# Kernel tuning notes

Measured on AMD Instinct MI355X. Metric: run time of the kernel, lower is better.

Reference implementation:

```python
import jax, jax.numpy as jnp
import numpy as np

B, S, E, HEADS = 2, 2048, 2048, 16


def setup_inputs() -> dict:
    key = jax.random.key(0)
    k1, k2, k3 = jax.random.split(key, 3)
    x = jax.random.normal(k1, (B, S, E), dtype=jnp.float32)
    # Linear weights stored as (in, out); torch uses y = x @ W.T with W (out, in) -- same math.
    W_qkvh = jax.random.normal(k2, (E, 3 * E + HEADS), dtype=jnp.float32) * (E ** -0.5)
    W_out = jax.random.normal(k3, (E, E), dtype=jnp.float32) * (E ** -0.5)
    return {"x": x, "W_qkvh": W_qkvh, "W_out": W_out}


def reference(x, W_qkvh, W_out):
    b, s, e = x.shape
    heads = W_qkvh.shape[1] - 3 * e
    d = e // heads
    scale = e ** 0.5

    proj = x @ W_qkvh                                  # (b, s, 3e + heads)
    QKV, Hg = proj[..., : 3 * e], proj[..., 3 * e:]
    Hg = jnp.tanh(Hg).transpose(0, 2, 1)[..., None]    # (b, h, s, 1) gate
    QKV = QKV.reshape(b, s, heads, 3 * d).transpose(0, 2, 1, 3)  # (b, h, s, 3d)
    Q, K, V = jnp.split(QKV, 3, axis=-1)               # each (b, h, s, d)

    # Cummean(H*K) along seq: cumsum(n * x) / n^2 with n = 1..s
    n = jnp.arange(1, s + 1, dtype=x.dtype).reshape(1, 1, s, 1)
    Kc = jnp.cumsum(n * (Hg * K), axis=2) / (n * n)    # (b, h, s, d)

    scores = jnp.einsum('bhqd,bhkd->bhqk', Q, Kc) / scale
    causal = jnp.triu(jnp.ones((s, s), dtype=bool), k=1)
    scores = jnp.where(causal, -jnp.inf, scores)
    attn = jax.nn.softmax(scores, axis=-1)

    out = jnp.einsum('bhqk,bhkd->bhqd', attn, V)       # (b, h, s, d)
    out = out.transpose(0, 2, 1, 3).reshape(b, s, e)
    return out @ W_out
```

## Files before the change

### kernel.cpp

```cpp
#include <hip/hip_runtime.h>
#include <hip/hip_bf16.h>
#include <math.h>

#define PB 2
#define PS 2048
#define PE 2048
#define PH 16
#define PD 128
#define PN_PROJ 6160
#define PM 4096
#define PQKV 6144

typedef __attribute__((ext_vector_type(8))) short bf16x8;
typedef __attribute__((ext_vector_type(4))) float f32x4;

__device__ __forceinline__ void gload_lds16(const void* g, void* l) {
  __builtin_amdgcn_global_load_lds((const __attribute__((address_space(1))) void*)g,
                                   (__attribute__((address_space(3))) void*)l, 16, 0, 0);
}

template <int BM, int BN, int WM, int WN, typename OutT>
__global__ __launch_bounds__(512, 1) void gemm_cs2(
    const __hip_bfloat16* __restrict__ A, const __hip_bfloat16* __restrict__ Bt,
    OutT* __restrict__ C, int K, int lda, int ldb, int ldc, int nTilesX) {
  constexpr int MF = BM / WM / 16;
  constexpr int NF = BN / WN / 16;
  constexpr int SLOT = (BM + BN) * 64;
  constexpr int AL = BM / 64;
  constexpr int BL = BN / 64;
  constexpr int NLD = AL + BL;

  __shared__ __align__(16) __hip_bfloat16 lds[2 * SLOT];

  const int tid = threadIdx.x;
  const int w = tid >> 6, lane = tid & 63;
  const int fq = lane >> 4, fr = lane & 15;
  const int wm = w / WN, wn = w % WN;

  const int total = gridDim.x;
  const int swz = (blockIdx.x & 7) * (total >> 3) + (blockIdx.x >> 3);
  const int mBase = (swz / nTilesX) * BM;
  const int nBase = (swz % nTilesX) * BN;

  const int srow = tid >> 3, sc = tid & 7;

  auto stage = [&](int t) {
    char* base = (char*)lds + (size_t)(t & 1) * SLOT * 2;
#pragma unroll
    for (int l = 0; l < AL; ++l) {
      int row = l * 64 + srow;
      int cs = sc ^ (row & 7);
      gload_lds16(A + (size_t)(mBase + row) * lda + t * 64 + cs * 8,
                  base + l * 8192 + w * 1024);
    }
#pragma unroll
    for (int l = 0; l < BL; ++l) {
      int row = l * 64 + srow;
      int cs = sc ^ (row & 7);
      gload_lds16(Bt + (size_t)(nBase + row) * ldb + t * 64 + cs * 8,
                  base + BM * 128 + l * 8192 + w * 1024);
    }
  };

  f32x4 acc[MF][NF];
#pragma unroll
  for (int m = 0; m < MF; ++m)
#pragma unroll
    for (int n = 0; n < NF; ++n) acc[m][n] = (f32x4){0.f, 0.f, 0.f, 0.f};

  const int NT = K / 64;
  stage(0); stage(1);

#pragma unroll 1
  for (int t = 0; t < NT; ++t) {
    if (t + 1 < NT) asm volatile("s_waitcnt vmcnt(%0)" ::"i"(NLD) : "memory");
    else            asm volatile("s_waitcnt vmcnt(0)" ::: "memory");
    __builtin_amdgcn_s_barrier();
    __builtin_amdgcn_sched_barrier(0);

    const __hip_bfloat16* sl = lds + (size_t)(t & 1) * SLOT;

    bf16x8 av[MF], bv[NF];
#pragma unroll
    for (int m = 0; m < MF; ++m) {
      int row = wm * (BM / WM) + m * 16 + fr;
      av[m] = *(const bf16x8*)&sl[row * 64 + ((fq ^ (row & 7)) * 8)];
    }
#pragma unroll
    for (int n = 0; n < NF; ++n) {
      int row = wn * (BN / WN) + n * 16 + fr;
      bv[n] = *(const bf16x8*)&sl[BM * 64 + row * 64 + ((fq ^ (row & 7)) * 8)];
    }
    asm volatile("s_waitcnt lgkmcnt(0)" ::: "memory");
    __builtin_amdgcn_sched_barrier(0);
    __builtin_amdgcn_s_setprio(1);
#pragma unroll
    for (int m = 0; m < MF; ++m)
#pragma unroll
      for (int n = 0; n < NF; ++n)
        acc[m][n] = __builtin_amdgcn_mfma_f32_16x16x32_bf16(av[m], bv[n], acc[m][n], 0, 0, 0);
    __builtin_amdgcn_s_setprio(0);

#pragma unroll
    for (int m = 0; m < MF; ++m) {
      int row = wm * (BM / WM) + m * 16 + fr;
      av[m] = *(const bf16x8*)&sl[row * 64 + (((4 + fq) ^ (row & 7)) * 8)];
    }
#pragma unroll
    for (int n = 0; n < NF; ++n) {
      int row = wn * (BN / WN) + n * 16 + fr;
      bv[n] = *(const bf16x8*)&sl[BM * 64 + row * 64 + (((4 + fq) ^ (row & 7)) * 8)];
    }
    asm volatile("s_waitcnt lgkmcnt(0)" ::: "memory");
    __builtin_amdgcn_s_barrier();
    __builtin_amdgcn_sched_barrier(0);
    if (t + 2 < NT) stage(t + 2);
    __builtin_amdgcn_s_setprio(1);
#pragma unroll
    for (int m = 0; m < MF; ++m)
#pragma unroll
      for (int n = 0; n < NF; ++n)
        acc[m][n] = __builtin_amdgcn_mfma_f32_16x16x32_bf16(av[m], bv[n], acc[m][n], 0, 0, 0);
    __builtin_amdgcn_s_setprio(0);
  }

#pragma unroll
  for (int m = 0; m < MF; ++m) {
#pragma unroll
    for (int n = 0; n < NF; ++n) {
      int row0 = mBase + wm * (BM / WM) + m * 16 + fq * 4;
      int col = nBase + wn * (BN / WN) + n * 16 + fr;
#pragma unroll
      for (int j = 0; j < 4; ++j) {
        if constexpr (__is_same(OutT, float))
          C[(size_t)(row0 + j) * ldc + col] = acc[m][n][j];
        else
          C[(size_t)(row0 + j) * ldc + col] = __float2bfloat16(acc[m][n][j]);
      }
    }
  }
}

template <int BM, int BN, int WM, int WN, typename OutT>
__global__ __launch_bounds__(512, 1) void gemm_cs3(
    const __hip_bfloat16* __restrict__ A, const __hip_bfloat16* __restrict__ Bt,
    OutT* __restrict__ C, int K, int lda, int ldb, int ldc, int nTilesX) {
  constexpr int MF = BM / WM / 16;
  constexpr int NF = BN / WN / 16;
  constexpr int SLOT = (BM + BN) * 64;
  constexpr int AL = BM / 64;
  constexpr int BL = BN / 64;
  constexpr int NLD = AL + BL;

  __shared__ __align__(16) __hip_bfloat16 lds[3 * SLOT];

  const int tid = threadIdx.x;
  const int w = tid >> 6, lane = tid & 63;
  const int fq = lane >> 4, fr = lane & 15;
  const int wm = w / WN, wn = w % WN;

  const int total = gridDim.x;
  const int swz = (blockIdx.x & 7) * (total >> 3) + (blockIdx.x >> 3);
  const int mBase = (swz / nTilesX) * BM;
  const int nBase = (swz % nTilesX) * BN;

  const int srow = tid >> 3, sc = tid & 7;

  auto stage = [&](int t) {
    char* base = (char*)lds + (size_t)(t % 3) * SLOT * 2;
#pragma unroll
    for (int l = 0; l < AL; ++l) {
      int row = l * 64 + srow;
      int cs = sc ^ (row & 7);
      gload_lds16(A + (size_t)(mBase + row) * lda + t * 64 + cs * 8,
                  base + l * 8192 + w * 1024);
    }
#pragma unroll
    for (int l = 0; l < BL; ++l) {
      int row = l * 64 + srow;
      int cs = sc ^ (row & 7);
      gload_lds16(Bt + (size_t)(nBase + row) * ldb + t * 64 + cs * 8,
                  base + BM * 128 + l * 8192 + w * 1024);
    }
  };

  f32x4 acc[MF][NF];
#pragma unroll
  for (int m = 0; m < MF; ++m)
#pragma unroll
    for (int n = 0; n < NF; ++n) acc[m][n] = (f32x4){0.f, 0.f, 0.f, 0.f};

  const int NT = K / 64;
  stage(0); stage(1);

#pragma unroll 1
  for (int t = 0; t < NT; ++t) {
    if (t + 1 < NT) asm volatile("s_waitcnt vmcnt(%0)" ::"i"(NLD) : "memory");
    else            asm volatile("s_waitcnt vmcnt(0)" ::: "memory");
    __builtin_amdgcn_s_barrier();
    __builtin_amdgcn_sched_barrier(0);
    if (t + 2 < NT) stage(t + 2);

    const __hip_bfloat16* sl = lds + (size_t)(t % 3) * SLOT;

#pragma unroll
    for (int kk = 0; kk < 2; ++kk) {
      bf16x8 av[MF], bv[NF];
#pragma unroll
      for (int m = 0; m < MF; ++m) {
        int row = wm * (BM / WM) + m * 16 + fr;
        av[m] = *(const bf16x8*)&sl[row * 64 + (((kk * 4 + fq) ^ (row & 7)) * 8)];
      }
#pragma unroll
      for (int n = 0; n < NF; ++n) {
        int row = wn * (BN / WN) + n * 16 + fr;
        bv[n] = *(const bf16x8*)&sl[BM * 64 + row * 64 + (((kk * 4 + fq) ^ (row & 7)) * 8)];
      }
      asm volatile("s_waitcnt lgkmcnt(0)" ::: "memory");
      __builtin_amdgcn_sched_barrier(0);
      __builtin_amdgcn_s_setprio(1);
#pragma unroll
      for (int m = 0; m < MF; ++m)
#pragma unroll
        for (int n = 0; n < NF; ++n)
          acc[m][n] = __builtin_amdgcn_mfma_f32_16x16x32_bf16(av[m], bv[n], acc[m][n], 0, 0, 0);
      __builtin_amdgcn_s_setprio(0);
    }
  }

#pragma unroll
  for (int m = 0; m < MF; ++m) {
#pragma unroll
    for (int n = 0; n < NF; ++n) {
      int row0 = mBase + wm * (BM / WM) + m * 16 + fq * 4;
      int col = nBase + wn * (BN / WN) + n * 16 + fr;
#pragma unroll
      for (int j = 0; j < 4; ++j) {
        if constexpr (__is_same(OutT, float))
          C[(size_t)(row0 + j) * ldc + col] = acc[m][n][j];
        else
          C[(size_t)(row0 + j) * ldc + col] = __float2bfloat16(acc[m][n][j]);
      }
    }
  }
}

__global__ __launch_bounds__(256) void cast_f32_bf16(const float* __restrict__ in,
                                                     __hip_bfloat16* __restrict__ out,
                                                     int n4) {
  int i = blockIdx.x * 256 + threadIdx.x;
  if (i >= n4) return;
  float4 v = ((const float4*)in)[i];
  union { __hip_bfloat16 h[4]; uint2 u; } pk;
  pk.h[0] = __float2bfloat16(v.x); pk.h[1] = __float2bfloat16(v.y);
  pk.h[2] = __float2bfloat16(v.z); pk.h[3] = __float2bfloat16(v.w);
  ((uint2*)out)[i] = pk.u;
}

__global__ __launch_bounds__(256) void transpose_cast(const float* __restrict__ W,
                                                      __hip_bfloat16* __restrict__ Wt,
                                                      int ldw, int ldt, int nOff) {
  __shared__ float t[32][33];
  int nb = blockIdx.x * 32, kb = blockIdx.y * 32;
  int tx = threadIdx.x & 31, ty = threadIdx.x >> 5;
#pragma unroll
  for (int i = 0; i < 4; ++i) {
    int k = ty + i * 8;
    t[k][tx] = W[(size_t)(kb + k) * ldw + nOff + nb + tx];
  }
  __syncthreads();
#pragma unroll
  for (int i = 0; i < 4; ++i) {
    int n = ty + i * 8;
    Wt[(size_t)(nb + n) * ldt + kb + tx] = __float2bfloat16(t[tx][n]);
  }
}

__global__ __launch_bounds__(256) void hg_from_x(const float* __restrict__ x,
                                                 const float* __restrict__ W,
                                                 float* __restrict__ hgbuf) {
  int bs = blockIdx.x;
  int b = bs >> 11, s = bs & (PS - 1);
  __shared__ float xs[PE];
  __shared__ float red[16][17];
  const float* xr = x + (size_t)bs * PE;
  for (int i = threadIdx.x; i < PE / 4; i += 256)
    *(float4*)&xs[i * 4] = ((const float4*)xr)[i];
  __syncthreads();
  int h = threadIdx.x & 15, part = threadIdx.x >> 4;
  float acc = 0.f;
  for (int k = part * 128; k < part * 128 + 128; ++k)
    acc += xs[k] * W[(size_t)k * PN_PROJ + 3 * PE + h];
  red[part][h] = acc;
  __syncthreads();
  if (threadIdx.x < 16) {
    float sm = 0.f;
#pragma unroll
    for (int p = 0; p < 16; ++p) sm += red[p][threadIdx.x];
    hgbuf[(size_t)(b * PH + threadIdx.x) * PS + s] = tanhf(sm);
  }
}

#define KC_SCALE 0.022097086912079608f

__global__ __launch_bounds__(128) void kc_pass1(const __hip_bfloat16* __restrict__ proj,
                                                const float* __restrict__ hgbuf,
                                                float* __restrict__ csum) {
  int c = blockIdx.x & 15, bh = blockIdx.x >> 4;
  int h = bh & (PH - 1), b = bh >> 4;
  int d = threadIdx.x;
  __shared__ float hgs[128];
  hgs[d] = hgbuf[bh * PS + c * 128 + d];
  __syncthreads();
  const __hip_bfloat16* kbase = proj + (size_t)(b * PS) * PQKV + h * 384 + 128 + d;
  float acc = 0.f;
  int j0 = c * 128;
  for (int i = 0; i < 128; ++i) {
    int j = j0 + i;
    acc += (float)(j + 1) * hgs[i] * __bfloat162float(kbase[(size_t)j * PQKV]);
  }
  csum[blockIdx.x * 128 + d] = acc;
}

__global__ __launch_bounds__(128) void kc_pass2(__hip_bfloat16* __restrict__ proj,
                                                const float* __restrict__ hgbuf,
                                                const float* __restrict__ csum) {
  int c = blockIdx.x & 15, bh = blockIdx.x >> 4;
  int h = bh & (PH - 1), b = bh >> 4;
  int d = threadIdx.x;
  __shared__ float hgs[128];
  hgs[d] = hgbuf[bh * PS + c * 128 + d];
  __syncthreads();
  float acc = 0.f;
  for (int cc = 0; cc < c; ++cc) acc += csum[(bh * 16 + cc) * 128 + d];
  __hip_bfloat16* kbase = proj + (size_t)(b * PS) * PQKV + h * 384 + 128 + d;
  int j0 = c * 128;
  for (int i = 0; i < 128; ++i) {
    int j = j0 + i;
    acc += (float)(j + 1) * hgs[i] * __bfloat162float(kbase[(size_t)j * PQKV]);
    float t = (float)(j + 1);
    kbase[(size_t)j * PQKV] = __float2bfloat16(acc / (t * t) * KC_SCALE);
  }
}

__global__ __launch_bounds__(256) void vt_pack(const __hip_bfloat16* __restrict__ proj,
                                               __hip_bfloat16* __restrict__ Vtp) {
  int sc = blockIdx.x & 31, bh = blockIdx.x >> 5;
  int b = bh >> 4, h = bh & 15;
  int s0 = sc * 64;
  int tid = threadIdx.x;
  __shared__ __align__(16) __hip_bfloat16 Vlds[64][136];
  const __hip_bfloat16* src = proj + (size_t)(b * PS + s0) * PQKV + h * 384 + 256;
#pragma unroll
  for (int it = 0; it < 4; ++it) {
    int i = it * 256 + tid;
    int row = i >> 4, ch = i & 15;
    *(bf16x8*)&Vlds[row][ch * 8] = *(const bf16x8*)&src[(size_t)row * PQKV + ch * 8];
  }
  __syncthreads();
  int d = tid >> 1, half = tid & 1;
  __hip_bfloat16* dst = Vtp + ((size_t)bh * 128 + d) * PS + s0 + half * 32;
#pragma unroll
  for (int c8 = 0; c8 < 8; ++c8) {
    union { __hip_bfloat16 h4[4]; uint2 u; } pk;
#pragma unroll
    for (int k = 0; k < 4; ++k) pk.h4[k] = Vlds[half * 32 + c8 * 4 + k][d];
    *(uint2*)&dst[c8 * 4] = pk.u;
  }
}

__global__ __launch_bounds__(256) void attn_mfma(const __hip_bfloat16* __restrict__ proj,
                                                 const __hip_bfloat16* __restrict__ Vtp,
                                                 __hip_bfloat16* __restrict__ O) {
  const int bid = (blockIdx.x & 7) * 32 + (blockIdx.x >> 3);
  const int bh = bid >> 3, pk = bid & 7;
  const int b = bh >> 4, h = bh & 15;
  const int tid = threadIdx.x;
  const int w = tid >> 6, lane = tid & 63;
  const int fq = lane >> 4, fr = lane & 15;

  __shared__ __align__(16) char smem[120832];
  __hip_bfloat16* Psw = (__hip_bfloat16*)(smem + 65536) + w * 32 * 72;
  __hip_bfloat16* Os = (__hip_bfloat16*)(smem + 84480);

  const __hip_bfloat16* kb0 = proj + (size_t)(b * PS) * PQKV + h * 384 + 128;
  const __hip_bfloat16* vb0 = Vtp + (size_t)bh * 128 * PS;

  const int klr = lane >> 4, kc = lane & 15;
  const int vlr = lane >> 3, vc = lane & 7;

  auto stageKV = [&](int t, int bufi) {
    char* ksb = smem + bufi * 16384;
    char* vsb = smem + 32768 + bufi * 16384;
    const __hip_bfloat16* kb = kb0 + (size_t)(t * 64) * PQKV;
    const __hip_bfloat16* vb = vb0 + t * 64;
#pragma unroll
    for (int p = 0; p < 4; ++p) {
      int row = w * 16 + p * 4 + klr;
      int cs = kc ^ (row & 7);
      gload_lds16(kb + (size_t)row * PQKV + cs * 8, ksb + (w * 16 + p * 4) * 256);
    }
#pragma unroll
    for (int p = 0; p < 4; ++p) {
      int row = w * 32 + p * 8 + vlr;
      int cs = vc ^ (row & 7);
      gload_lds16(vb + (size_t)row * PS + cs * 8, vsb + (w * 32 + p * 8) * 128);
    }
  };

  stageKV(0, 0);
  int cur = 0;

#pragma unroll 1
  for (int phase = 0; phase < 2; ++phase) {
    const int qt = (phase == 0) ? pk : 15 - pk;
    const int nt = (qt + 1) * 2;
    const int q0 = qt * 128;
    const int qw = q0 + w * 32;

    const __hip_bfloat16* qbase = proj + (size_t)(b * PS + qw) * PQKV + h * 384;
    bf16x8 qf[2][4];
#pragma unroll
    for (int r2 = 0; r2 < 2; ++r2)
#pragma unroll
      for (int kk = 0; kk < 4; ++kk)
        qf[r2][kk] = *(const bf16x8*)&qbase[(size_t)(r2 * 16 + fr) * PQKV + kk * 32 + fq * 8];

    f32x4 oacc[2][8];
#pragma unroll
    for (int r2 = 0; r2 < 2; ++r2)
#pragma unroll
      for (int nd = 0; nd < 8; ++nd) oacc[r2][nd] = (f32x4){0.f, 0.f, 0.f, 0.f};
    float m_[2] = {-__builtin_inff(), -__builtin_inff()};
    float l_[2] = {0.f, 0.f};

#pragma unroll 1
    for (int kt = 0; kt < nt; ++kt) {
      const bool hasNext = (kt + 1 < nt) || (phase == 0);
      if (hasNext) stageKV((kt + 1 < nt) ? kt + 1 : 0, cur ^ 1);

      if (kt * 64 <= qw + 31) {
        const __hip_bfloat16* Ks = (const __hip_bfloat16*)(smem + cur * 16384);
        const __hip_bfloat16* Vts = (const __hip_bfloat16*)(smem + 32768 + cur * 16384);
        const bool diag = (kt * 64 + 63) > qw;

        f32x4 sacc[2][4];
#pragma unroll
        for (int r2 = 0; r2 < 2; ++r2)
#pragma unroll
          for (int n = 0; n < 4; ++n) sacc[r2][n] = (f32x4){0.f, 0.f, 0.f, 0.f};
#pragma unroll
        for (int kk = 0; kk < 4; ++kk) {
#pragma unroll
          for (int n = 0; n < 4; ++n) {
            bf16x8 kf = *(const bf16x8*)&Ks[(n * 16 + fr) * 128 + (((kk * 4 + fq) ^ (fr & 7)) * 8)];
            sacc[0][n] = __builtin_amdgcn_mfma_f32_16x16x32_bf16(kf, qf[0][kk], sacc[0][n], 0, 0, 0);
            sacc[1][n] = __builtin_amdgcn_mfma_f32_16x16x32_bf16(kf, qf[1][kk], sacc[1][n], 0, 0, 0);
          }
        }

#pragma unroll
        for (int r2 = 0; r2 < 2; ++r2) {
          const int qg = qw + r2 * 16 + fr;
          float sv[4][4];
#pragma unroll
          for (int n = 0; n < 4; ++n)
#pragma unroll
            for (int j = 0; j < 4; ++j) {
              float s = sacc[r2][n][j];
              if (diag && (kt * 64 + n * 16 + fq * 4 + j) > qg) s = -__builtin_inff();
              sv[n][j] = s;
            }
          float pmax = sv[0][0];
#pragma unroll
          for (int n = 0; n < 4; ++n)
#pragma unroll
            for (int j = 0; j < 4; ++j) pmax = fmaxf(pmax, sv[n][j]);
          pmax = fmaxf(pmax, __shfl_xor(pmax, 16, 64));
          pmax = fmaxf(pmax, __shfl_xor(pmax, 32, 64));

          const bool nof = __all(pmax <= m_[r2] + 8.f);
          const float mn = nof ? m_[r2] : fmaxf(m_[r2], pmax);
          float ps = 0.f;
#pragma unroll
          for (int n = 0; n < 4; ++n) {
            union { __hip_bfloat16 hh[4]; uint2 u; } pkk;
#pragma unroll
            for (int j = 0; j < 4; ++j) {
              float p = __expf(sv[n][j] - mn);
              ps += p;
              pkk.hh[j] = __float2bfloat16(p);
            }
            *(uint2*)&Psw[(r2 * 16 + fr) * 72 + n * 16 + fq * 4] = pkk.u;
          }
          ps += __shfl_xor(ps, 16, 64);
          ps += __shfl_xor(ps, 32, 64);

          if (!nof) {
            const float alpha = __expf(m_[r2] - mn);
            l_[r2] = l_[r2] * alpha + ps;
            m_[r2] = mn;
            float a0 = __shfl(alpha, fq * 4 + 0, 64);
            float a1 = __shfl(alpha, fq * 4 + 1, 64);
            float a2 = __shfl(alpha, fq * 4 + 2, 64);
            float a3 = __shfl(alpha, fq * 4 + 3, 64);
#pragma unroll
            for (int nd = 0; nd < 8; ++nd) {
              oacc[r2][nd][0] *= a0; oacc[r2][nd][1] *= a1;
              oacc[r2][nd][2] *= a2; oacc[r2][nd][3] *= a3;
            }
          } else {
            l_[r2] += ps;
          }
        }

#pragma unroll
        for (int kk2 = 0; kk2 < 2; ++kk2) {
          bf16x8 pa0 = *(const bf16x8*)&Psw[(0 * 16 + fr) * 72 + kk2 * 32 + fq * 8];
          bf16x8 pa1 = *(const bf16x8*)&Psw[(1 * 16 + fr) * 72 + kk2 * 32 + fq * 8];
#pragma unroll
          for (int nd = 0; nd < 8; ++nd) {
            bf16x8 vf = *(const bf16x8*)&Vts[(nd * 16 + fr) * 64 + (((kk2 * 4 + fq) ^ (fr & 7)) * 8)];
            oacc[0][nd] = __builtin_amdgcn_mfma_f32_16x16x32_bf16(pa0, vf, oacc[0][nd], 0, 0, 0);
            oacc[1][nd] = __builtin_amdgcn_mfma_f32_16x16x32_bf16(pa1, vf, oacc[1][nd], 0, 0, 0);
          }
        }
      }

      __syncthreads();
      cur ^= 1;
    }

    float i0 = 1.0f / l_[0], i1 = 1.0f / l_[1];
    float inv4[2][4];
#pragma unroll
    for (int j = 0; j < 4; ++j) {
      inv4[0][j] = __shfl(i0, fq * 4 + j, 64);
      inv4[1][j] = __shfl(i1, fq * 4 + j, 64);
    }
#pragma unroll
    for (int r2 = 0; r2 < 2; ++r2)
#pragma unroll
      for (int nd = 0; nd < 8; ++nd)
#pragma unroll
        for (int j = 0; j < 4; ++j)
          Os[(w * 32 + r2 * 16 + fq * 4 + j) * 136 + nd * 16 + fr] =
              __float2bfloat16(oacc[r2][nd][j] * inv4[r2][j]);
    __syncthreads();
#pragma unroll
    for (int it = 0; it < 8; ++it) {
      int i = it * 256 + tid;
      int row = i >> 4, ch = i & 15;
      *(bf16x8*)&O[(size_t)(b * PS + q0 + row) * PE + h * 128 + ch * 8] =
          *(const bf16x8*)&Os[row * 136 + ch * 8];
    }
  }
}

extern "C" void kernel_launch(void* const* d_in, const int* in_sizes, int n_in,
                              void* d_out, int out_size, void* d_ws, size_t ws_size,
                              hipStream_t stream) {
  const float* x     = (const float*)d_in[0];
  const float* Wqkvh = (const float*)d_in[1];
  const float* Wout  = (const float*)d_in[2];
  float* out = (float*)d_out;

  char* wsb = (char*)d_ws;
  __hip_bfloat16* proj = (__hip_bfloat16*)wsb;
  wsb += (size_t)PM * PQKV * 2;
  __hip_bfloat16* xb = (__hip_bfloat16*)wsb;
  wsb += (size_t)PM * PE * 2;
  __hip_bfloat16* Wq_t = (__hip_bfloat16*)wsb;
  wsb += (size_t)PQKV * PE * 2;
  __hip_bfloat16* Wout_t = (__hip_bfloat16*)wsb;
  wsb += (size_t)PE * PE * 2;
  __hip_bfloat16* Vtp = (__hip_bfloat16*)wsb;
  wsb += (size_t)PB * PH * PD * PS * 2;
  float* hgbuf = (float*)wsb;
  wsb += (size_t)PB * PH * PS * 4;
  float* csum = (float*)wsb;

  cast_f32_bf16<<<(PM * PE / 4 + 255) / 256, 256, 0, stream>>>(x, xb, PM * PE / 4);
  transpose_cast<<<dim3(PQKV / 32, PE / 32), 256, 0, stream>>>(Wqkvh, Wq_t, PN_PROJ, PE, 0);
  transpose_cast<<<dim3(PE / 32, PE / 32), 256, 0, stream>>>(Wout, Wout_t, PE, PE, 0);

  gemm_cs2<128, 384, 2, 4, __hip_bfloat16>
      <<<dim3((PM / 128) * (PQKV / 384)), 512, 0, stream>>>(
          xb, Wq_t, proj, PE, PE, PE, PQKV, PQKV / 384);

  hg_from_x<<<PM, 256, 0, stream>>>(x, Wqkvh, hgbuf);
  kc_pass1<<<PB * PH * 16, 128, 0, stream>>>(proj, hgbuf, csum);
  kc_pass2<<<PB * PH * 16, 128, 0, stream>>>(proj, hgbuf, csum);

  vt_pack<<<PB * PH * 32, 256, 0, stream>>>(proj, Vtp);
  __hip_bfloat16* Ob = xb;
  attn_mfma<<<PB * PH * 8, 256, 0, stream>>>(proj, Vtp, Ob);

  gemm_cs3<128, 256, 2, 4, float>
      <<<dim3((PM / 128) * (PE / 256)), 512, 0, stream>>>(
          Ob, Wout_t, out, PE, PE, PE, PE, PE / 256);
}
```

Baseline: 319.5 us.

## Replace QKV projection GEMM with 256x256 tile, four-phase ping-pong MFMA schedule

The QKV projection GEMM moves from a 128x384 tile to a 256x256 tile whose per-warp 128x64 sub-tile is processed in four quadrants. LDS fragment loads for the next quadrant are interleaved with MFMA bursts, separated by block barriers and setprio, in a ping-pong style. The aim is to raise arithmetic intensity per LDS byte and overlap LDS reads with matrix math. It uses the full 128KB of LDS and more barriers per k-step. The grid shrinks to 384 blocks, which may fill the CUs less evenly.

```diff
diff --git a/kernel.cpp b/kernel.cpp
--- a/kernel.cpp
+++ b/kernel.cpp
@@ -19,117 +19,150 @@
                                    (__attribute__((address_space(3))) void*)l, 16, 0, 0);
 }
 
-template <int BM, int BN, int WM, int WN, typename OutT>
-__global__ __launch_bounds__(512, 1) void gemm_cs2(
+template <typename OutT>
+__global__ __launch_bounds__(512, 1) void gemm_8p(
     const __hip_bfloat16* __restrict__ A, const __hip_bfloat16* __restrict__ Bt,
     OutT* __restrict__ C, int K, int lda, int ldb, int ldc, int nTilesX) {
-  constexpr int MF = BM / WM / 16;
-  constexpr int NF = BN / WN / 16;
-  constexpr int SLOT = (BM + BN) * 64;
-  constexpr int AL = BM / 64;
-  constexpr int BL = BN / 64;
-  constexpr int NLD = AL + BL;
-
-  __shared__ __align__(16) __hip_bfloat16 lds[2 * SLOT];
+  __shared__ __align__(16) char lds[131072];
 
   const int tid = threadIdx.x;
   const int w = tid >> 6, lane = tid & 63;
   const int fq = lane >> 4, fr = lane & 15;
-  const int wm = w / WN, wn = w % WN;
+  const int wm = w >> 2, wn = w & 3;
 
   const int total = gridDim.x;
   const int swz = (blockIdx.x & 7) * (total >> 3) + (blockIdx.x >> 3);
-  const int mBase = (swz / nTilesX) * BM;
-  const int nBase = (swz % nTilesX) * BN;
+  const int mBase = (swz / nTilesX) * 256;
+  const int nBase = (swz % nTilesX) * 256;
 
   const int srow = tid >> 3, sc = tid & 7;
 
   auto stage = [&](int t) {
-    char* base = (char*)lds + (size_t)(t & 1) * SLOT * 2;
-#pragma unroll
-    for (int l = 0; l < AL; ++l) {
+    char* base = lds + (size_t)(t & 1) * 65536;
+#pragma unroll
+    for (int l = 0; l < 4; ++l) {
       int row = l * 64 + srow;
       int cs = sc ^ (row & 7);
       gload_lds16(A + (size_t)(mBase + row) * lda + t * 64 + cs * 8,
                   base + l * 8192 + w * 1024);
     }
 #pragma unroll
-    for (int l = 0; l < BL; ++l) {
+    for (int l = 0; l < 4; ++l) {
       int row = l * 64 + srow;
       int cs = sc ^ (row & 7);
       gload_lds16(Bt + (size_t)(nBase + row) * ldb + t * 64 + cs * 8,
-                  base + BM * 128 + l * 8192 + w * 1024);
+                  base + 32768 + l * 8192 + w * 1024);
     }
   };
 
-  f32x4 acc[MF][NF];
-#pragma unroll
-  for (int m = 0; m < MF; ++m)
-#pragma unroll
-    for (int n = 0; n < NF; ++n) acc[m][n] = (f32x4){0.f, 0.f, 0.f, 0.f};
+  f32x4 acc[8][4];
+#pragma unroll
+  for (int m = 0; m < 8; ++m)
+#pragma unroll
+    for (int n = 0; n < 4; ++n) acc[m][n] = (f32x4){0.f, 0.f, 0.f, 0.f};
 
   const int NT = K / 64;
   stage(0); stage(1);
 
 #pragma unroll 1
   for (int t = 0; t < NT; ++t) {
-    if (t + 1 < NT) asm volatile("s_waitcnt vmcnt(%0)" ::"i"(NLD) : "memory");
+    if (t + 1 < NT) asm volatile("s_waitcnt vmcnt(8)" ::: "memory");
     else            asm volatile("s_waitcnt vmcnt(0)" ::: "memory");
     __builtin_amdgcn_s_barrier();
     __builtin_amdgcn_sched_barrier(0);
 
-    const __hip_bfloat16* sl = lds + (size_t)(t & 1) * SLOT;
-
-    bf16x8 av[MF], bv[NF];
-#pragma unroll
-    for (int m = 0; m < MF; ++m) {
-      int row = wm * (BM / WM) + m * 16 + fr;
-      av[m] = *(const bf16x8*)&sl[row * 64 + ((fq ^ (row & 7)) * 8)];
-    }
-#pragma unroll
-    for (int n = 0; n < NF; ++n) {
-      int row = wn * (BN / WN) + n * 16 + fr;
-      bv[n] = *(const bf16x8*)&sl[BM * 64 + row * 64 + ((fq ^ (row & 7)) * 8)];
-    }
+    const __hip_bfloat16* slA = (const __hip_bfloat16*)(lds + (size_t)(t & 1) * 65536);
+    const __hip_bfloat16* slB = slA + 16384;
+
+    bf16x8 avA[4][2], bv01[2][2], bv23[2][2], avB[4][2];
+#pragma unroll
+    for (int m = 0; m < 4; ++m)
+#pragma unroll
+      for (int kk = 0; kk < 2; ++kk) {
+        int row = wm * 128 + m * 16 + fr;
+        avA[m][kk] = *(const bf16x8*)&slA[row * 64 + (((kk * 4 + fq) ^ (row & 7)) * 8)];
+      }
+#pragma unroll
+    for (int n = 0; n < 2; ++n)
+#pragma unroll
+      for (int kk = 0; kk < 2; ++kk) {
+        int row = wn * 64 + n * 16 + fr;
+        bv01[n][kk] = *(const bf16x8*)&slB[row * 64 + (((kk * 4 + fq) ^ (row & 7)) * 8)];
+      }
+    __builtin_amdgcn_s_barrier();
     asm volatile("s_waitcnt lgkmcnt(0)" ::: "memory");
     __builtin_amdgcn_sched_barrier(0);
     __builtin_amdgcn_s_setprio(1);
 #pragma unroll
-    for (int m = 0; m < MF; ++m)
-#pragma unroll
-      for (int n = 0; n < NF; ++n)
-        acc[m][n] = __builtin_amdgcn_mfma_f32_16x16x32_bf16(av[m], bv[n], acc[m][n], 0, 0, 0);
+    for (int m = 0; m < 4; ++m)
+#pragma unroll
+      for (int n = 0; n < 2; ++n)
+#pragma unroll
+        for (int kk = 0; kk < 2; ++kk)
+          acc[m][n] = __builtin_amdgcn_mfma_f32_16x16x32_bf16(avA[m][kk], bv01[n][kk], acc[m][n], 0, 0, 0);
     __builtin_amdgcn_s_setprio(0);
-
-#pragma unroll
-    for (int m = 0; m < MF; ++m) {
-      int row = wm * (BM / WM) + m * 16 + fr;
-      av[m] = *(const bf16x8*)&sl[row * 64 + (((4 + fq) ^ (row & 7)) * 8)];
-    }
-#pragma unroll
-    for (int n = 0; n < NF; ++n) {
-      int row = wn * (BN / WN) + n * 16 + fr;
-      bv[n] = *(const bf16x8*)&sl[BM * 64 + row * 64 + (((4 + fq) ^ (row & 7)) * 8)];
-    }
+    __builtin_amdgcn_s_barrier();
+
+#pragma unroll
+    for (int n = 0; n < 2; ++n)
+#pragma unroll
+      for (int kk = 0; kk < 2; ++kk) {
+        int row = wn * 64 + (2 + n) * 16 + fr;
+        bv23[n][kk] = *(const bf16x8*)&slB[row * 64 + (((kk * 4 + fq) ^ (row & 7)) * 8)];
+      }
+    __builtin_amdgcn_s_barrier();
     asm volatile("s_waitcnt lgkmcnt(0)" ::: "memory");
-    __builtin_amdgcn_s_barrier();
     __builtin_amdgcn_sched_barrier(0);
+    __builtin_amdgcn_s_setprio(1);
+#pragma unroll
+    for (int m = 0; m < 4; ++m)
+#pragma unroll
+      for (int n = 0; n < 2; ++n)
+#pragma unroll
+        for (int kk = 0; kk < 2; ++kk)
+          acc[m][2 + n] = __builtin_amdgcn_mfma_f32_16x16x32_bf16(avA[m][kk], bv23[n][kk], acc[m][2 + n], 0, 0, 0);
+    __builtin_amdgcn_s_setprio(0);
+    __builtin_amdgcn_s_barrier();
+
+#pragma unroll
+    for (int m = 0; m < 4; ++m)
+#pragma unroll
+      for (int kk = 0; kk < 2; ++kk) {
+        int row = wm * 128 + (4 + m) * 16 + fr;
+        avB[m][kk] = *(const bf16x8*)&slA[row * 64 + (((kk * 4 + fq) ^ (row & 7)) * 8)];
+      }
+    __builtin_amdgcn_s_barrier();
+    asm volatile("s_waitcnt lgkmcnt(0)" ::: "memory");
+    __builtin_amdgcn_sched_barrier(0);
+    __builtin_amdgcn_s_setprio(1);
+#pragma unroll
+    for (int m = 0; m < 4; ++m)
+#pragma unroll
+      for (int n = 0; n < 2; ++n)
+#pragma unroll
+        for (int kk = 0; kk < 2; ++kk)
+          acc[4 + m][2 + n] = __builtin_amdgcn_mfma_f32_16x16x32_bf16(avB[m][kk], bv23[n][kk], acc[4 + m][2 + n], 0, 0, 0);
+    __builtin_amdgcn_s_setprio(0);
+    __builtin_amdgcn_s_barrier();
+
     if (t + 2 < NT) stage(t + 2);
     __builtin_amdgcn_s_setprio(1);
 #pragma unroll
-    for (int m = 0; m < MF; ++m)
-#pragma unroll
-      for (int n = 0; n < NF; ++n)
-        acc[m][n] = __builtin_amdgcn_mfma_f32_16x16x32_bf16(av[m], bv[n], acc[m][n], 0, 0, 0);
+    for (int m = 0; m < 4; ++m)
+#pragma unroll
+      for (int n = 0; n < 2; ++n)
+#pragma unroll
+        for (int kk = 0; kk < 2; ++kk)
+          acc[4 + m][n] = __builtin_amdgcn_mfma_f32_16x16x32_bf16(avB[m][kk], bv01[n][kk], acc[4 + m][n], 0, 0, 0);
     __builtin_amdgcn_s_setprio(0);
   }
 
 #pragma unroll
-  for (int m = 0; m < MF; ++m) {
-#pragma unroll
-    for (int n = 0; n < NF; ++n) {
-      int row0 = mBase + wm * (BM / WM) + m * 16 + fq * 4;
-      int col = nBase + wn * (BN / WN) + n * 16 + fr;
+  for (int m = 0; m < 8; ++m) {
+#pragma unroll
+    for (int n = 0; n < 4; ++n) {
+      int row0 = mBase + wm * 128 + m * 16 + fq * 4;
+      int col = nBase + wn * 64 + n * 16 + fr;
 #pragma unroll
       for (int j = 0; j < 4; ++j) {
         if constexpr (__is_same(OutT, float))
@@ -584,9 +617,9 @@
   transpose_cast<<<dim3(PQKV / 32, PE / 32), 256, 0, stream>>>(Wqkvh, Wq_t, PN_PROJ, PE, 0);
   transpose_cast<<<dim3(PE / 32, PE / 32), 256, 0, stream>>>(Wout, Wout_t, PE, PE, 0);
 
-  gemm_cs2<128, 384, 2, 4, __hip_bfloat16>
-      <<<dim3((PM / 128) * (PQKV / 384)), 512, 0, stream>>>(
-          xb, Wq_t, proj, PE, PE, PE, PQKV, PQKV / 384);
+  gemm_8p<__hip_bfloat16>
+      <<<dim3((PM / 256) * (PQKV / 256)), 512, 0, stream>>>(
+          xb, Wq_t, proj, PE, PE, PE, PQKV, PQKV / 256);
 
   hg_from_x<<<PM, 256, 0, stream>>>(x, Wqkvh, hgbuf);
   kc_pass1<<<PB * PH * 16, 128, 0, stream>>>(proj, hgbuf, csum);
```

Result: slower. 341.5 us (+6.9%).

## Write QKV projection head-major and fold x bf16 cast into gate kernel

Applied to the files above, without the earlier changes.

The QKV GEMM epilogue now scatters results into separate head-major Q, K and V buffers laid out (b,h,s,d), replacing the interleaved (b*s, 3E) projection matrix. Downstream kernels (cumsum passes, V transpose, attention) read contiguous 256-byte rows instead of rows strided by 6144 elements. Separately, the standalone f32-to-bf16 cast of x is removed and done inside hg_from_x, which already loads x into shared memory, saving one launch and one read of x. The GEMM epilogue store now has a per-element head/batch index computation and writes to three destinations.

```diff
diff --git a/kernel.cpp b/kernel.cpp
--- a/kernel.cpp
+++ b/kernel.cpp
@@ -9,7 +9,6 @@
 #define PD 128
 #define PN_PROJ 6160
 #define PM 4096
-#define PQKV 6144
 
 typedef __attribute__((ext_vector_type(8))) short bf16x8;
 typedef __attribute__((ext_vector_type(4))) float f32x4;
@@ -19,10 +18,11 @@
                                    (__attribute__((address_space(3))) void*)l, 16, 0, 0);
 }
 
-template <int BM, int BN, int WM, int WN, typename OutT>
-__global__ __launch_bounds__(512, 1) void gemm_cs2(
+__global__ __launch_bounds__(512, 1) void gemm_qkv(
     const __hip_bfloat16* __restrict__ A, const __hip_bfloat16* __restrict__ Bt,
-    OutT* __restrict__ C, int K, int lda, int ldb, int ldc, int nTilesX) {
+    __hip_bfloat16* __restrict__ Qp, __hip_bfloat16* __restrict__ Kp,
+    __hip_bfloat16* __restrict__ Vp, int K, int nTilesX) {
+  constexpr int BM = 128, BN = 384, WM = 2, WN = 4;
   constexpr int MF = BM / WM / 16;
   constexpr int NF = BN / WN / 16;
   constexpr int SLOT = (BM + BN) * 64;
@@ -40,7 +40,8 @@
   const int total = gridDim.x;
   const int swz = (blockIdx.x & 7) * (total >> 3) + (blockIdx.x >> 3);
   const int mBase = (swz / nTilesX) * BM;
-  const int nBase = (swz % nTilesX) * BN;
+  const int h = swz % nTilesX;
+  const int nBase = h * BN;
 
   const int srow = tid >> 3, sc = tid & 7;
 
@@ -50,14 +51,14 @@
     for (int l = 0; l < AL; ++l) {
       int row = l * 64 + srow;
       int cs = sc ^ (row & 7);
-      gload_lds16(A + (size_t)(mBase + row) * lda + t * 64 + cs * 8,
+      gload_lds16(A + (size_t)(mBase + row) * K + t * 64 + cs * 8,
                   base + l * 8192 + w * 1024);
     }
 #pragma unroll
     for (int l = 0; l < BL; ++l) {
       int row = l * 64 + srow;
       int cs = sc ^ (row & 7);
-      gload_lds16(Bt + (size_t)(nBase + row) * ldb + t * 64 + cs * 8,
+      gload_lds16(Bt + (size_t)(nBase + row) * K + t * 64 + cs * 8,
                   base + BM * 128 + l * 8192 + w * 1024);
     }
   };
@@ -129,13 +130,15 @@
 #pragma unroll
     for (int n = 0; n < NF; ++n) {
       int row0 = mBase + wm * (BM / WM) + m * 16 + fq * 4;
-      int col = nBase + wn * (BN / WN) + n * 16 + fr;
+      int colL = wn * (BN / WN) + n * 16 + fr;
+      int which = colL >> 7;
+      int d = colL & 127;
+      __hip_bfloat16* dst = which == 0 ? Qp : (which == 1 ? Kp : Vp);
 #pragma unroll
       for (int j = 0; j < 4; ++j) {
-        if constexpr (__is_same(OutT, float))
-          C[(size_t)(row0 + j) * ldc + col] = acc[m][n][j];
-        else
-          C[(size_t)(row0 + j) * ldc + col] = __float2bfloat16(acc[m][n][j]);
+        int row = row0 + j;
+        int b = row >> 11, s = row & (PS - 1);
+        dst[(((size_t)(b * PH + h)) * PS + s) * PD + d] = __float2bfloat16(acc[m][n][j]);
       }
     }
   }
@@ -245,18 +248,6 @@
   }
 }
 
-__global__ __launch_bounds__(256) void cast_f32_bf16(const float* __restrict__ in,
-                                                     __hip_bfloat16* __restrict__ out,
-                                                     int n4) {
-  int i = blockIdx.x * 256 + threadIdx.x;
-  if (i >= n4) return;
-  float4 v = ((const float4*)in)[i];
-  union { __hip_bfloat16 h[4]; uint2 u; } pk;
-  pk.h[0] = __float2bfloat16(v.x); pk.h[1] = __float2bfloat16(v.y);
-  pk.h[2] = __float2bfloat16(v.z); pk.h[3] = __float2bfloat16(v.w);
-  ((uint2*)out)[i] = pk.u;
-}
-
 __global__ __launch_bounds__(256) void transpose_cast(const float* __restrict__ W,
                                                       __hip_bfloat16* __restrict__ Wt,
                                                       int ldw, int ldt, int nOff) {
@@ -278,7 +269,8 @@
 
 __global__ __launch_bounds__(256) void hg_from_x(const float* __restrict__ x,
                                                  const float* __restrict__ W,
-                                                 float* __restrict__ hgbuf) {
+                                                 float* __restrict__ hgbuf,
+                                                 __hip_bfloat16* __restrict__ xb) {
   int bs = blockIdx.x;
   int b = bs >> 11, s = bs & (PS - 1);
   __shared__ float xs[PE];
@@ -287,6 +279,12 @@
   for (int i = threadIdx.x; i < PE / 4; i += 256)
     *(float4*)&xs[i * 4] = ((const float4*)xr)[i];
   __syncthreads();
+  {
+    union { __hip_bfloat16 hh[8]; bf16x8 v; } pk;
+#pragma unroll
+    for (int k = 0; k < 8; ++k) pk.hh[k] = __float2bfloat16(xs[threadIdx.x * 8 + k]);
+    *(bf16x8*)&xb[(size_t)bs * PE + threadIdx.x * 8] = pk.v;
+  }
   int h = threadIdx.x & 15, part = threadIdx.x >> 4;
   float acc = 0.f;
   for (int k = part * 128; k < part * 128 + 128; ++k)
@@ -303,63 +301,57 @@
 
 #define KC_SCALE 0.022097086912079608f
 
-__global__ __launch_bounds__(128) void kc_pass1(const __hip_bfloat16* __restrict__ proj,
+__global__ __launch_bounds__(128) void kc_pass1(const __hip_bfloat16* __restrict__ Kp,
                                                 const float* __restrict__ hgbuf,
                                                 float* __restrict__ csum) {
   int c = blockIdx.x & 15, bh = blockIdx.x >> 4;
-  int h = bh & (PH - 1), b = bh >> 4;
   int d = threadIdx.x;
   __shared__ float hgs[128];
-  hgs[d] = hgbuf[bh * PS + c * 128 + d];
+  hgs[d] = hgbuf[(size_t)bh * PS + c * 128 + d];
   __syncthreads();
-  const __hip_bfloat16* kbase = proj + (size_t)(b * PS) * PQKV + h * 384 + 128 + d;
+  const __hip_bfloat16* kb = Kp + ((size_t)bh * PS + c * 128) * PD + d;
   float acc = 0.f;
   int j0 = c * 128;
-  for (int i = 0; i < 128; ++i) {
-    int j = j0 + i;
-    acc += (float)(j + 1) * hgs[i] * __bfloat162float(kbase[(size_t)j * PQKV]);
-  }
+  for (int i = 0; i < 128; ++i)
+    acc += (float)(j0 + i + 1) * hgs[i] * __bfloat162float(kb[(size_t)i * PD]);
   csum[blockIdx.x * 128 + d] = acc;
 }
 
-__global__ __launch_bounds__(128) void kc_pass2(__hip_bfloat16* __restrict__ proj,
+__global__ __launch_bounds__(128) void kc_pass2(__hip_bfloat16* __restrict__ Kp,
                                                 const float* __restrict__ hgbuf,
                                                 const float* __restrict__ csum) {
   int c = blockIdx.x & 15, bh = blockIdx.x >> 4;
-  int h = bh & (PH - 1), b = bh >> 4;
   int d = threadIdx.x;
   __shared__ float hgs[128];
-  hgs[d] = hgbuf[bh * PS + c * 128 + d];
+  hgs[d] = hgbuf[(size_t)bh * PS + c * 128 + d];
   __syncthreads();
   float acc = 0.f;
   for (int cc = 0; cc < c; ++cc) acc += csum[(bh * 16 + cc) * 128 + d];
-  __hip_bfloat16* kbase = proj + (size_t)(b * PS) * PQKV + h * 384 + 128 + d;
+  __hip_bfloat16* kb = Kp + ((size_t)bh * PS + c * 128) * PD + d;
   int j0 = c * 128;
   for (int i = 0; i < 128; ++i) {
-    int j = j0 + i;
-    acc += (float)(j + 1) * hgs[i] * __bfloat162float(kbase[(size_t)j * PQKV]);
-    float t = (float)(j + 1);
-    kbase[(size_t)j * PQKV] = __float2bfloat16(acc / (t * t) * KC_SCALE);
-  }
-}
-
-__global__ __launch_bounds__(256) void vt_pack(const __hip_bfloat16* __restrict__ proj,
+    float t = (float)(j0 + i + 1);
+    acc += t * hgs[i] * __bfloat162float(kb[(size_t)i * PD]);
+    kb[(size_t)i * PD] = __float2bfloat16(acc / (t * t) * KC_SCALE);
+  }
+}
+
+__global__ __launch_bounds__(256) void vt_pack(const __hip_bfloat16* __restrict__ Vp,
                                                __hip_bfloat16* __restrict__ Vtp) {
   int sc = blockIdx.x & 31, bh = blockIdx.x >> 5;
-  int b = bh >> 4, h = bh & 15;
   int s0 = sc * 64;
   int tid = threadIdx.x;
   __shared__ __align__(16) __hip_bfloat16 Vlds[64][136];
-  const __hip_bfloat16* src = proj + (size_t)(b * PS + s0) * PQKV + h * 384 + 256;
+  const __hip_bfloat16* src = Vp + ((size_t)bh * PS + s0) * PD;
 #pragma unroll
   for (int it = 0; it < 4; ++it) {
     int i = it * 256 + tid;
     int row = i >> 4, ch = i & 15;
-    *(bf16x8*)&Vlds[row][ch * 8] = *(const bf16x8*)&src[(size_t)row * PQKV + ch * 8];
+    *(bf16x8*)&Vlds[row][ch * 8] = *(const bf16x8*)&src[(size_t)row * PD + ch * 8];
   }
   __syncthreads();
   int d = tid >> 1, half = tid & 1;
-  __hip_bfloat16* dst = Vtp + ((size_t)bh * 128 + d) * PS + s0 + half * 32;
+  __hip_bfloat16* dst = Vtp + ((size_t)bh * PD + d) * PS + s0 + half * 32;
 #pragma unroll
   for (int c8 = 0; c8 < 8; ++c8) {
     union { __hip_bfloat16 h4[4]; uint2 u; } pk;
@@ -369,7 +361,8 @@
   }
 }
 
-__global__ __launch_bounds__(256) void attn_mfma(const __hip_bfloat16* __restrict__ proj,
+__global__ __launch_bounds__(256) void attn_mfma(const __hip_bfloat16* __restrict__ Qp,
+                                                 const __hip_bfloat16* __restrict__ Kp,
                                                  const __hip_bfloat16* __restrict__ Vtp,
                                                  __hip_bfloat16* __restrict__ O) {
   const int bid = (blockIdx.x & 7) * 32 + (blockIdx.x >> 3);
@@ -383,8 +376,8 @@
   __hip_bfloat16* Psw = (__hip_bfloat16*)(smem + 65536) + w * 32 * 72;
   __hip_bfloat16* Os = (__hip_bfloat16*)(smem + 84480);
 
-  const __hip_bfloat16* kb0 = proj + (size_t)(b * PS) * PQKV + h * 384 + 128;
-  const __hip_bfloat16* vb0 = Vtp + (size_t)bh * 128 * PS;
+  const __hip_bfloat16* kb0 = Kp + (size_t)bh * PS * PD;
+  const __hip_bfloat16* vb0 = Vtp + (size_t)bh * PD * PS;
 
   const int klr = lane >> 4, kc = lane & 15;
   const int vlr = lane >> 3, vc = lane & 7;
@@ -392,13 +385,13 @@
   auto stageKV = [&](int t, int bufi) {
     char* ksb = smem + bufi * 16384;
     char* vsb = smem + 32768 + bufi * 16384;
-    const __hip_bfloat16* kb = kb0 + (size_t)(t * 64) * PQKV;
+    const __hip_bfloat16* kb = kb0 + (size_t)(t * 64) * PD;
     const __hip_bfloat16* vb = vb0 + t * 64;
 #pragma unroll
     for (int p = 0; p < 4; ++p) {
       int row = w * 16 + p * 4 + klr;
       int cs = kc ^ (row & 7);
-      gload_lds16(kb + (size_t)row * PQKV + cs * 8, ksb + (w * 16 + p * 4) * 256);
+      gload_lds16(kb + (size_t)row * PD + cs * 8, ksb + (w * 16 + p * 4) * 256);
     }
 #pragma unroll
     for (int p = 0; p < 4; ++p) {
@@ -418,13 +411,13 @@
     const int q0 = qt * 128;
     const int qw = q0 + w * 32;
 
-    const __hip_bfloat16* qbase = proj + (size_t)(b * PS + qw) * PQKV + h * 384;
+    const __hip_bfloat16* qbase = Qp + ((size_t)bh * PS + qw) * PD;
     bf16x8 qf[2][4];
 #pragma unroll
     for (int r2 = 0; r2 < 2; ++r2)
 #pragma unroll
       for (int kk = 0; kk < 4; ++kk)
-        qf[r2][kk] = *(const bf16x8*)&qbase[(size_t)(r2 * 16 + fr) * PQKV + kk * 32 + fq * 8];
+        qf[r2][kk] = *(const bf16x8*)&qbase[(size_t)(r2 * 16 + fr) * PD + kk * 32 + fq * 8];
 
     f32x4 oacc[2][8];
 #pragma unroll
@@ -565,36 +558,30 @@
   const float* Wout  = (const float*)d_in[2];
   float* out = (float*)d_out;
 
+  const size_t HD = (size_t)PB * PH * PS * PD;
   char* wsb = (char*)d_ws;
-  __hip_bfloat16* proj = (__hip_bfloat16*)wsb;
-  wsb += (size_t)PM * PQKV * 2;
-  __hip_bfloat16* xb = (__hip_bfloat16*)wsb;
-  wsb += (size_t)PM * PE * 2;
-  __hip_bfloat16* Wq_t = (__hip_bfloat16*)wsb;
-  wsb += (size_t)PQKV * PE * 2;
-  __hip_bfloat16* Wout_t = (__hip_bfloat16*)wsb;
-  wsb += (size_t)PE * PE * 2;
-  __hip_bfloat16* Vtp = (__hip_bfloat16*)wsb;
-  wsb += (size_t)PB * PH * PD * PS * 2;
-  float* hgbuf = (float*)wsb;
-  wsb += (size_t)PB * PH * PS * 4;
+  __hip_bfloat16* Qp = (__hip_bfloat16*)wsb;   wsb += HD * 2;
+  __hip_bfloat16* Kp = (__hip_bfloat16*)wsb;   wsb += HD * 2;
+  __hip_bfloat16* Vp = (__hip_bfloat16*)wsb;   wsb += HD * 2;
+  __hip_bfloat16* Vtp = (__hip_bfloat16*)wsb;  wsb += HD * 2;
+  __hip_bfloat16* xb = (__hip_bfloat16*)wsb;   wsb += (size_t)PM * PE * 2;
+  __hip_bfloat16* Wq_t = (__hip_bfloat16*)wsb; wsb += (size_t)3 * PE * PE * 2;
+  __hip_bfloat16* Wout_t = (__hip_bfloat16*)wsb; wsb += (size_t)PE * PE * 2;
+  float* hgbuf = (float*)wsb;                  wsb += (size_t)PB * PH * PS * 4;
   float* csum = (float*)wsb;
 
-  cast_f32_bf16<<<(PM * PE / 4 + 255) / 256, 256, 0, stream>>>(x, xb, PM * PE / 4);
-  transpose_cast<<<dim3(PQKV / 32, PE / 32), 256, 0, stream>>>(Wqkvh, Wq_t, PN_PROJ, PE, 0);
+  hg_from_x<<<PM, 256, 0, stream>>>(x, Wqkvh, hgbuf, xb);
+  transpose_cast<<<dim3(3 * PE / 32, PE / 32), 256, 0, stream>>>(Wqkvh, Wq_t, PN_PROJ, PE, 0);
   transpose_cast<<<dim3(PE / 32, PE / 32), 256, 0, stream>>>(Wout, Wout_t, PE, PE, 0);
 
-  gemm_cs2<128, 384, 2, 4, __hip_bfloat16>
-      <<<dim3((PM / 128) * (PQKV / 384)), 512, 0, stream>>>(
-          xb, Wq_t, proj, PE, PE, PE, PQKV, PQKV / 384);
-
-  hg_from_x<<<PM, 256, 0, stream>>>(x, Wqkvh, hgbuf);
-  kc_pass1<<<PB * PH * 16, 128, 0, stream>>>(proj, hgbuf, csum);
-  kc_pass2<<<PB * PH * 16, 128, 0, stream>>>(proj, hgbuf, csum);
-
-  vt_pack<<<PB * PH * 32, 256, 0, stream>>>(proj, Vtp);
+  gemm_qkv<<<dim3((PM / 128) * PH), 512, 0, stream>>>(xb, Wq_t, Qp, Kp, Vp, PE, PH);
+
+  kc_pass1<<<PB * PH * 16, 128, 0, stream>>>(Kp, hgbuf, csum);
+  kc_pass2<<<PB * PH * 16, 128, 0, stream>>>(Kp, hgbuf, csum);
+
+  vt_pack<<<PB * PH * 32, 256, 0, stream>>>(Vp, Vtp);
   __hip_bfloat16* Ob = xb;
-  attn_mfma<<<PB * PH * 8, 256, 0, stream>>>(proj, Vtp, Ob);
+  attn_mfma<<<PB * PH * 8, 256, 0, stream>>>(Qp, Kp, Vtp, Ob);
 
   gemm_cs3<128, 256, 2, 4, float>
       <<<dim3((PM / 128) * (PE / 256)), 512, 0, stream>>>(
```

New measurement: 313.2 us. No clear change (-1.9%).
